# Optimization experiments

Hardware: AMD Instinct MI355X
Metric: run time of the kernel (lower is better)

Reference implementation:

```python
import jax, jax.numpy as jnp
import numpy as np

B, N, D = 16, 512, 256
PH, UH, UPH = 8, 4, 4          # P_GAT heads, U_GAT heads, UP_GAT heads
P_LAYERS, U_LAYERS = 2, 1
FH, NC = 128, 2                # final hidden, num classes
N_TRAIT = 4


def setup_inputs() -> dict:
    key = jax.random.key(0)
    keys = iter(jax.random.split(key, 64))

    def rn(shape, s=0.05):
        return jax.random.normal(next(keys), shape, dtype=jnp.float32) * s

    inp = {
        "p_mask": jnp.ones((B, N), jnp.float32),
        "feature": rn((B, N, D), 1.0),
        "c_node": rn((B, 1, D), 1.0),
        "pgat_W": rn((D, D)),
        "pgat_attn": rn((PH, 2 * (D // PH))),
    }
    for i in range(1, 5):
        inp[f"up{i}_qw"] = rn((D, D))
        inp[f"up{i}_qb"] = rn((D,))
        inp[f"up{i}_kw"] = rn((D, D))
        inp[f"up{i}_kb"] = rn((D,))
        inp[f"up{i}_ow"] = rn((D, D * UPH))
        inp[f"up{i}_ob"] = rn((D,))
    inp["ugat_W"] = rn((D, D))
    inp["ugat_attn"] = rn((UH, 2 * (D // UH)))
    inp["mlp_w1"] = rn((FH, D))
    inp["mlp_b1"] = rn((FH,))
    inp["mlp_w2"] = rn((FH, FH))
    inp["mlp_b2"] = rn((FH,))
    for i in range(1, 5):
        inp[f"fcf{i}_w"] = rn((NC, FH))
        inp[f"fcf{i}_b"] = rn((NC,))
    return inp


def _mh_gat(feature, W, attn_w, n_head, num_layers, adj=None):
    """Shared math of P_GAT / U_GAT.
    attn(cat([q_i, k_j]))[..., h, h] decomposes into q_i.wq_h + k_j.wk_h,
    identical math to the broadcast-concat-linear-diagonal in the source."""
    Bx, Nx, d = feature.shape
    dh = d // n_head
    wq, wk = attn_w[:, :dh], attn_w[:, dh:]           # [h, dh] each
    for _ in range(num_layers):
        qk = (feature @ W.T).reshape(Bx, Nx, n_head, dh)
        sq = jnp.einsum('bqhd,hd->bqh', qk, wq)
        sk = jnp.einsum('bkhd,hd->bkh', qk, wk)
        scores = jnp.tanh(sq[:, :, None, :] + sk[:, None, :, :])  # [B,q,k,h]
        if adj is not None:
            scores = jnp.where(adj[:, :, :, None] == 0, jnp.float32(-1e-8), scores)
        att = jax.nn.softmax(scores, axis=-2)          # softmax over k
        hid = jnp.tanh(jnp.einsum('bqkh,bkhd->bqhd', att, qk))
        feature = feature + hid.reshape(Bx, Nx, d)
    return feature


def _up_gat(p_mask, p_feat, u_feat, qw, qb, kw, kb, ow, ob):
    """UP_GAT: all heads/layers share params & inputs -> identical heads."""
    d = p_feat.shape[-1]
    q = u_feat @ qw.T + qb                             # [B,1,D]
    k = p_feat @ kw.T + kb                             # [B,Np,D]
    sim = jnp.einsum('bqd,bkd->bqk', q, k) / jnp.sqrt(jnp.float32(d))
    sim = jnp.where(p_mask[:, None, :] == 0, jnp.float32(1e-8), sim)
    att = jax.nn.softmax(sim, axis=2)
    head = att @ p_feat                                # [B,1,D]
    mh = jnp.concatenate([head] * UPH, axis=-1)        # concat of identical heads
    return (mh @ ow.T + ob)[:, 0, :]                   # squeeze(1)


def reference(p_mask, feature, c_node, pgat_W, pgat_attn,
              up1_qw, up1_qb, up1_kw, up1_kb, up1_ow, up1_ob,
              up2_qw, up2_qb, up2_kw, up2_kb, up2_ow, up2_ob,
              up3_qw, up3_qb, up3_kw, up3_kb, up3_ow, up3_ob,
              up4_qw, up4_qb, up4_kw, up4_kb, up4_ow, up4_ob,
              ugat_W, ugat_attn, mlp_w1, mlp_b1, mlp_w2, mlp_b2,
              fcf1_w, fcf1_b, fcf2_w, fcf2_b, fcf3_w, fcf3_b, fcf4_w, fcf4_b):
    Bx = p_mask.shape[0]
    adj = p_mask[:, :, None] * p_mask[:, None, :]      # [B,N,N]
    new_p = _mh_gat(feature, pgat_W, pgat_attn, PH, P_LAYERS, adj=adj)
    new_mask = jnp.concatenate([p_mask, jnp.ones((Bx, 1), p_mask.dtype)], axis=1)
    comb = jnp.concatenate([new_p, c_node], axis=1)    # [B,N+1,D]

    u1 = _up_gat(new_mask, comb, c_node, up1_qw, up1_qb, up1_kw, up1_kb, up1_ow, up1_ob)
    u2 = _up_gat(new_mask, comb, c_node, up2_qw, up2_qb, up2_kw, up2_kb, up2_ow, up2_ob)
    u3 = _up_gat(new_mask, comb, c_node, up3_qw, up3_qb, up3_kw, up3_kb, up3_ow, up3_ob)
    u4 = _up_gat(new_mask, comb, c_node, up4_qw, up4_qb, up4_kw, up4_kb, up4_ow, up4_ob)

    u = jnp.stack([u1, u2, u3, u4], axis=1)            # [B,4,D]
    u = _mh_gat(u, ugat_W, ugat_attn, UH, U_LAYERS, adj=None)

    def mlp(x):  # fcs1..4 share modules in the torch source
        h = jax.nn.relu(x @ mlp_w1.T + mlp_b1)
        return jax.nn.relu(h @ mlp_w2.T + mlp_b2)

    heads = [(fcf1_w, fcf1_b), (fcf2_w, fcf2_b), (fcf3_w, fcf3_b), (fcf4_w, fcf4_b)]
    logits = [mlp(u[:, i]) @ w.T + b for i, (w, b) in enumerate(heads)]
    return jnp.stack(logits, axis=0)                   # [4,B,NC]
```

## Files before the change

kernel.cpp:

```cpp
#include <hip/hip_runtime.h>

constexpr int CB   = 16;
constexpr int CN   = 512;
constexpr int CD   = 256;
constexpr int CPH  = 8;
constexpr int CDH  = 32;
constexpr int CNP1 = 513;
constexpr int CFH  = 128;
constexpr int CNC  = 2;

typedef __bf16 bf16x8 __attribute__((ext_vector_type(8)));
typedef __bf16 bf16x4 __attribute__((ext_vector_type(4)));
typedef float  f32x4  __attribute__((ext_vector_type(4)));

__device__ __forceinline__ float tanh_fast(float x) {
  x = fminf(fmaxf(x, -15.f), 15.f);
  float e = __expf(2.f * x);
  return (e - 1.f) / (e + 1.f);
}

__global__ __launch_bounds__(256) void gemm_fused(
    const float* __restrict__ A, const float* __restrict__ W,
    const float* __restrict__ attnw, __bf16* __restrict__ C,
    float* __restrict__ sqT, float* __restrict__ skT)
{
  const int t  = threadIdx.x;
  const int nt = blockIdx.x * 64;
  const int mt = blockIdx.y * 64;
  const int wv = t >> 6, ln = t & 63;
  const int quad = ln >> 4, lc = ln & 15;

  __shared__ __align__(16) __bf16 aHi[64][56];
  __shared__ __align__(16) __bf16 aLo[64][56];
  __shared__ __align__(16) __bf16 bHi[64][56];
  __shared__ __align__(16) __bf16 bLo[64][56];

  f32x4 acc[4];
#pragma unroll
  for (int j = 0; j < 4; j++)
#pragma unroll
    for (int r = 0; r < 4; r++) acc[j][r] = 0.f;

  const int sr  = t >> 2;
  const int skq = (t & 3) * 8;

  for (int k0 = 0; k0 < 256; k0 += 32) {
    __syncthreads();
    {
      const float* ap = A + (size_t)(mt + sr) * 256 + k0 + skq;
      const float* wp = W + (size_t)(nt + sr) * 256 + k0 + skq;
      float4 a0 = *(const float4*)ap, a1 = *(const float4*)(ap + 4);
      float4 w0 = *(const float4*)wp, w1 = *(const float4*)(wp + 4);
      float av[8] = {a0.x, a0.y, a0.z, a0.w, a1.x, a1.y, a1.z, a1.w};
      float wvv[8] = {w0.x, w0.y, w0.z, w0.w, w1.x, w1.y, w1.z, w1.w};
      bf16x8 ah, al, bh, bl;
#pragma unroll
      for (int j = 0; j < 8; j++) {
        ah[j] = (__bf16)av[j];
        al[j] = (__bf16)(av[j] - (float)ah[j]);
        bh[j] = (__bf16)wvv[j];
        bl[j] = (__bf16)(wvv[j] - (float)bh[j]);
      }
      *(bf16x8*)&aHi[sr][skq] = ah;
      *(bf16x8*)&aLo[sr][skq] = al;
      *(bf16x8*)&bHi[sr][skq] = bh;
      *(bf16x8*)&bLo[sr][skq] = bl;
    }
    __syncthreads();
    bf16x8 fah = *(const bf16x8*)&aHi[wv * 16 + lc][quad * 8];
    bf16x8 fal = *(const bf16x8*)&aLo[wv * 16 + lc][quad * 8];
#pragma unroll
    for (int j = 0; j < 4; j++) {
      bf16x8 fbh = *(const bf16x8*)&bHi[j * 16 + lc][quad * 8];
      bf16x8 fbl = *(const bf16x8*)&bLo[j * 16 + lc][quad * 8];
      acc[j] = __builtin_amdgcn_mfma_f32_16x16x32_bf16(fah, fbh, acc[j], 0, 0, 0);
      acc[j] = __builtin_amdgcn_mfma_f32_16x16x32_bf16(fah, fbl, acc[j], 0, 0, 0);
      acc[j] = __builtin_amdgcn_mfma_f32_16x16x32_bf16(fal, fbh, acc[j], 0, 0, 0);
    }
  }
#pragma unroll
  for (int j = 0; j < 4; j++)
#pragma unroll
    for (int r = 0; r < 4; r++)
      C[(size_t)(mt + wv * 16 + quad * 4 + r) * 256 + nt + j * 16 + lc] =
          (__bf16)acc[j][r];

  const int hA = blockIdx.x * 2, hB = hA + 1;
  const float wqa0 = attnw[hA * 64 + lc],      wqa1 = attnw[hA * 64 + 16 + lc];
  const float wka0 = attnw[hA * 64 + 32 + lc], wka1 = attnw[hA * 64 + 48 + lc];
  const float wqb0 = attnw[hB * 64 + lc],      wqb1 = attnw[hB * 64 + 16 + lc];
  const float wkb0 = attnw[hB * 64 + 32 + lc], wkb1 = attnw[hB * 64 + 48 + lc];
  float sqa[4], ska[4], sqb[4], skb[4];
#pragma unroll
  for (int r = 0; r < 4; r++) {
    sqa[r] = acc[0][r] * wqa0 + acc[1][r] * wqa1;
    ska[r] = acc[0][r] * wka0 + acc[1][r] * wka1;
    sqb[r] = acc[2][r] * wqb0 + acc[3][r] * wqb1;
    skb[r] = acc[2][r] * wkb0 + acc[3][r] * wkb1;
  }
#pragma unroll
  for (int m = 1; m <= 8; m <<= 1) {
#pragma unroll
    for (int r = 0; r < 4; r++) {
      sqa[r] += __shfl_xor(sqa[r], m);
      ska[r] += __shfl_xor(ska[r], m);
      sqb[r] += __shfl_xor(sqb[r], m);
      skb[r] += __shfl_xor(skb[r], m);
    }
  }
  if (lc == 0) {
#pragma unroll
    for (int r = 0; r < 4; r++) {
      int gm = mt + wv * 16 + quad * 4 + r;
      int bb = gm >> 9, nn = gm & 511;
      sqT[((size_t)bb * CPH + hA) * CN + nn] = sqa[r];
      skT[((size_t)bb * CPH + hA) * CN + nn] = ska[r];
      sqT[((size_t)bb * CPH + hB) * CN + nn] = sqb[r];
      skT[((size_t)bb * CPH + hB) * CN + nn] = skb[r];
    }
  }
}

__global__ __launch_bounds__(256) void pgat_attn_mfma(
    const __bf16* __restrict__ qk, const float* __restrict__ sqT,
    const float* __restrict__ skT, const float* __restrict__ pmask,
    const float* __restrict__ fin, float* __restrict__ fout, int outStride)
{
  const int qt = blockIdx.x;
  const int h  = blockIdx.y;
  const int b  = blockIdx.z;
  const int t  = threadIdx.x;
  const int wv = t >> 6;
  const int ln = t & 63;
  const int quad = ln >> 4;
  const int lc   = ln & 15;

  __shared__ __align__(16) __bf16 pbuf[64][72];
  __shared__ __align__(16) __bf16 vbuf[32][72];
  __shared__ float skl[CN];
  __shared__ float pml[CN];
  __shared__ float sql[64];
  __shared__ float pmq[64];

  for (int i = t; i < CN; i += 256) {
    skl[i] = skT[((size_t)b * CPH + h) * CN + i];
    pml[i] = pmask[b * CN + i];
  }
  if (t < 64) {
    sql[t] = sqT[((size_t)b * CPH + h) * CN + qt * 64 + t];
    pmq[t] = pmask[b * CN + qt * 64 + t];
  }

  f32x4 accV0 = {0.f, 0.f, 0.f, 0.f};
  f32x4 accV1 = {0.f, 0.f, 0.f, 0.f};
  f32x4 accD  = {0.f, 0.f, 0.f, 0.f};
  bf16x8 ones;
#pragma unroll
  for (int j = 0; j < 8; j++) ones[j] = (__bf16)1.0f;

  const int qg = t >> 2;
  const int kb = (t & 3) * 16;
  const int vkk = t >> 3;
  const int vdq = (t & 7) * 4;

  for (int k0 = 0; k0 < CN; k0 += 64) {
    __syncthreads();
    {
      bf16x4 v0 = *(const bf16x4*)(qk + ((size_t)(b * CN + k0 + vkk)) * CD + h * CDH + vdq);
      bf16x4 v1 = *(const bf16x4*)(qk + ((size_t)(b * CN + k0 + 32 + vkk)) * CD + h * CDH + vdq);
      vbuf[vdq + 0][vkk] = v0[0]; vbuf[vdq + 1][vkk] = v0[1];
      vbuf[vdq + 2][vkk] = v0[2]; vbuf[vdq + 3][vkk] = v0[3];
      vbuf[vdq + 0][32 + vkk] = v1[0]; vbuf[vdq + 1][32 + vkk] = v1[1];
      vbuf[vdq + 2][32 + vkk] = v1[2]; vbuf[vdq + 3][32 + vkk] = v1[3];
    }
    {
      float sq_ = sql[qg];
      float mq  = pmq[qg];
      bf16x8 w0, w1;
#pragma unroll
      for (int j = 0; j < 8; j++) {
        float s = tanh_fast(sq_ + skl[k0 + kb + j]);
        if (mq * pml[k0 + kb + j] == 0.f) s = -1e-8f;
        w0[j] = (__bf16)__expf(s);
      }
#pragma unroll
      for (int j = 0; j < 8; j++) {
        float s = tanh_fast(sq_ + skl[k0 + kb + 8 + j]);
        if (mq * pml[k0 + kb + 8 + j] == 0.f) s = -1e-8f;
        w1[j] = (__bf16)__expf(s);
      }
      *(bf16x8*)&pbuf[qg][kb]     = w0;
      *(bf16x8*)&pbuf[qg][kb + 8] = w1;
    }
    __syncthreads();
#pragma unroll
    for (int s = 0; s < 2; s++) {
      bf16x8 a  = *(const bf16x8*)&pbuf[wv * 16 + lc][s * 32 + quad * 8];
      bf16x8 b0 = *(const bf16x8*)&vbuf[lc][s * 32 + quad * 8];
      bf16x8 b1 = *(const bf16x8*)&vbuf[16 + lc][s * 32 + quad * 8];
      accV0 = __builtin_amdgcn_mfma_f32_16x16x32_bf16(a, b0, accV0, 0, 0, 0);
      accV1 = __builtin_amdgcn_mfma_f32_16x16x32_bf16(a, b1, accV1, 0, 0, 0);
      accD  = __builtin_amdgcn_mfma_f32_16x16x32_bf16(a, ones, accD, 0, 0, 0);
    }
  }
#pragma unroll
  for (int r = 0; r < 4; r++) {
    int q = qt * 64 + wv * 16 + quad * 4 + r;
    float inv = 1.f / accD[r];
    int d0 = h * CDH + lc;
    const float* ip = fin + ((size_t)b * CN + q) * CD;
    float*       op = fout + ((size_t)b * outStride + q) * CD;
    op[d0]      = ip[d0]      + tanh_fast(accV0[r] * inv);
    op[d0 + 16] = ip[d0 + 16] + tanh_fast(accV1[r] * inv);
  }
}


__global__ __launch_bounds__(256) void up_q_all(
    const float* __restrict__ cnode,
    const float* __restrict__ qw0, const float* __restrict__ qb0,
    const float* __restrict__ kw0, const float* __restrict__ kb0,
    const float* __restrict__ qw1, const float* __restrict__ qb1,
    const float* __restrict__ kw1, const float* __restrict__ kb1,
    const float* __restrict__ qw2, const float* __restrict__ qb2,
    const float* __restrict__ kw2, const float* __restrict__ kb2,
    const float* __restrict__ qw3, const float* __restrict__ qb3,
    const float* __restrict__ kw3, const float* __restrict__ kb3,
    float* __restrict__ qt_, float* __restrict__ qkb,
    float* __restrict__ comb, float* __restrict__ head, float* __restrict__ den)
{
  const int up = blockIdx.x, b = blockIdx.y, t = threadIdx.x;
  const float* qw = (up == 0) ? qw0 : (up == 1) ? qw1 : (up == 2) ? qw2 : qw3;
  const float* qb = (up == 0) ? qb0 : (up == 1) ? qb1 : (up == 2) ? qb2 : qb3;
  const float* kw = (up == 0) ? kw0 : (up == 1) ? kw1 : (up == 2) ? kw2 : kw3;
  const float* kb = (up == 0) ? kb0 : (up == 1) ? kb1 : (up == 2) ? kb2 : kb3;
  __shared__ float cl[CD];
  __shared__ float ql[CD];
  __shared__ float red[256];
  cl[t] = cnode[b * CD + t];
  head[((size_t)b * 4 + up) * CD + t] = 0.f;
  if (t == 0) den[b * 4 + up] = 0.f;
  __syncthreads();
  if (up == 0) comb[((size_t)b * CNP1 + CN) * CD + t] = cl[t];
  {
    const float* wr = qw + (size_t)t * CD;
    float a = qb[t];
#pragma unroll 4
    for (int k = 0; k < CD; k += 4) {
      float4 w4 = *(const float4*)(wr + k);
      a += cl[k] * w4.x + cl[k + 1] * w4.y + cl[k + 2] * w4.z + cl[k + 3] * w4.w;
    }
    ql[t] = a;
  }
  __syncthreads();
  {
    float a = 0.f;
    for (int d = 0; d < CD; d++) a += ql[d] * kw[d * CD + t];
    qt_[((size_t)up * CB + b) * CD + t] = a;
  }
  red[t] = ql[t] * kb[t];
  __syncthreads();
  for (int s = 128; s > 0; s >>= 1) { if (t < s) red[t] += red[t + s]; __syncthreads(); }
  if (t == 0) qkb[up * CB + b] = red[0];
}

__global__ __launch_bounds__(256) void up_headsim(
    const float* __restrict__ comb, const float* __restrict__ qt,
    const float* __restrict__ qkb, const float* __restrict__ pmask,
    float* __restrict__ head, float* __restrict__ den)
{
  const int b = blockIdx.x, n0 = blockIdx.y * 64, t = threadIdx.x;
  const int up = t >> 6, j = t & 63;
  __shared__ float qtl[4][CD];
  __shared__ float qkbl[4];
  __shared__ float attl[4][64];
  for (int i = t; i < 4 * CD; i += 256)
    qtl[i >> 8][i & 255] = qt[((size_t)(i >> 8) * CB + b) * CD + (i & 255)];
  if (t < 4) qkbl[t] = qkb[t * CB + b];
  __syncthreads();
  {
    const int n = n0 + j;
    float e = 0.f;
    if (n < CNP1) {
      const float* cr = comb + ((size_t)b * CNP1 + n) * CD;
      float p = 0.f;
#pragma unroll 4
      for (int d = 0; d < CD; d += 4) {
        float4 c4 = *(const float4*)(cr + d);
        p += qtl[up][d] * c4.x + qtl[up][d + 1] * c4.y
           + qtl[up][d + 2] * c4.z + qtl[up][d + 3] * c4.w;
      }
      float s = (p + qkbl[up]) * 0.0625f;
      float m = (n < CN) ? pmask[b * CN + n] : 1.f;
      if (m == 0.f) s = 1e-8f;
      e = __expf(s);
    }
    attl[up][j] = e;
  }
  __syncthreads();
  float4 acc = make_float4(0.f, 0.f, 0.f, 0.f);
  const int nmax = min(64, CNP1 - n0);
  for (int jj = 0; jj < nmax; jj++) {
    float a = attl[up][jj];
    float4 c4 = *(const float4*)(comb + ((size_t)b * CNP1 + n0 + jj) * CD + j * 4);
    acc.x += a * c4.x; acc.y += a * c4.y; acc.z += a * c4.z; acc.w += a * c4.w;
  }
  float* hp = head + ((size_t)b * 4 + up) * CD + j * 4;
  atomicAdd(hp + 0, acc.x); atomicAdd(hp + 1, acc.y);
  atomicAdd(hp + 2, acc.z); atomicAdd(hp + 3, acc.w);
  if (j == 0) {
    float s = 0.f;
    for (int jj = 0; jj < 64; jj++) s += attl[up][jj];
    atomicAdd(den + b * 4 + up, s);
  }
}

__global__ __launch_bounds__(256) void up_out_all(
    const float* __restrict__ head, const float* __restrict__ den,
    const float* __restrict__ ow0, const float* __restrict__ ob0,
    const float* __restrict__ ow1, const float* __restrict__ ob1,
    const float* __restrict__ ow2, const float* __restrict__ ob2,
    const float* __restrict__ ow3, const float* __restrict__ ob3,
    float* __restrict__ uout)
{
  const int b = blockIdx.x, up = blockIdx.y, t = threadIdx.x;
  const float* ow = (up == 0) ? ow0 : (up == 1) ? ow1 : (up == 2) ? ow2 : ow3;
  const float* ob = (up == 0) ? ob0 : (up == 1) ? ob1 : (up == 2) ? ob2 : ob3;
  __shared__ float hl[CD];
  hl[t] = head[((size_t)b * 4 + up) * CD + t] * (1.f / den[b * 4 + up]);
  __syncthreads();
  const float* r0 = ow + (size_t)t * 4 * CD;
  float a = ob[t];
#pragma unroll 2
  for (int dd = 0; dd < CD; dd += 4) {
    float4 w0 = *(const float4*)(r0 + dd);
    float4 w1 = *(const float4*)(r0 + CD + dd);
    float4 w2 = *(const float4*)(r0 + 2 * CD + dd);
    float4 w3 = *(const float4*)(r0 + 3 * CD + dd);
    a += hl[dd]     * (w0.x + w1.x + w2.x + w3.x)
       + hl[dd + 1] * (w0.y + w1.y + w2.y + w3.y)
       + hl[dd + 2] * (w0.z + w1.z + w2.z + w3.z)
       + hl[dd + 3] * (w0.w + w1.w + w2.w + w3.w);
  }
  uout[((size_t)b * 4 + up) * CD + t] = a;
}

__global__ __launch_bounds__(256) void ugat_qk(
    const float* __restrict__ u, const float* __restrict__ W,
    const float* __restrict__ attnw,
    float* __restrict__ uqk, float* __restrict__ sqk)
{
  const int b = blockIdx.x, node = blockIdx.y, t = threadIdx.x;
  __shared__ float ul[CD];
  __shared__ float qkl[CD];
  ul[t] = u[((size_t)b * 4 + node) * CD + t];
  __syncthreads();
  const float* wr = W + (size_t)t * CD;
  float p0 = 0.f, p1 = 0.f, p2 = 0.f, p3 = 0.f;
#pragma unroll 4
  for (int d = 0; d < CD; d += 16) {
    float4 w0 = *(const float4*)(wr + d);
    float4 w1 = *(const float4*)(wr + d + 4);
    float4 w2 = *(const float4*)(wr + d + 8);
    float4 w3 = *(const float4*)(wr + d + 12);
    p0 += ul[d +  0] * w0.x + ul[d +  1] * w0.y + ul[d +  2] * w0.z + ul[d +  3] * w0.w;
    p1 += ul[d +  4] * w1.x + ul[d +  5] * w1.y + ul[d +  6] * w1.z + ul[d +  7] * w1.w;
    p2 += ul[d +  8] * w2.x + ul[d +  9] * w2.y + ul[d + 10] * w2.z + ul[d + 11] * w2.w;
    p3 += ul[d + 12] * w3.x + ul[d + 13] * w3.y + ul[d + 14] * w3.z + ul[d + 15] * w3.w;
  }
  float a = (p0 + p1) + (p2 + p3);
  qkl[t] = a;
  uqk[((size_t)b * 4 + node) * CD + t] = a;
  __syncthreads();
  if (t < 8) {
    const int h = t >> 1, which = t & 1;
    const float* w = attnw + h * 128 + which * 64;
    float s = 0.f;
    for (int j = 0; j < 64; j++) s += qkl[h * 64 + j] * w[j];
    sqk[(((size_t)b * 4 + node) * 4 + h) * 2 + which] = s;
  }
}

__global__ __launch_bounds__(256) void ugat_mlp2(
    const float* __restrict__ u, const float* __restrict__ uqk,
    const float* __restrict__ sqk,
    const float* __restrict__ w1, const float* __restrict__ b1,
    const float* __restrict__ w2, const float* __restrict__ b2,
    const float* __restrict__ f1w, const float* __restrict__ f1b,
    const float* __restrict__ f2w, const float* __restrict__ f2b,
    const float* __restrict__ f3w, const float* __restrict__ f3b,
    const float* __restrict__ f4w, const float* __restrict__ f4b,
    float* __restrict__ out)
{
  const int b = blockIdx.x, trait = blockIdx.y, t = threadIdx.x;
  __shared__ float uq[4][CD];
  __shared__ float sl[4][4], kl[4][4];
  __shared__ float xl[CD];
  __shared__ float h1[CFH];
  __shared__ float h2[CFH];
  for (int i = t; i < 4 * CD; i += 256) uq[i >> 8][i & 255] = uqk[(size_t)b * 4 * CD + i];
  if (t < 16) {
    int node = t >> 2, h = t & 3;
    sl[node][h] = sqk[(((size_t)b * 4 + node) * 4 + h) * 2 + 0];
    kl[node][h] = sqk[(((size_t)b * 4 + node) * 4 + h) * 2 + 1];
  }
  float ur = u[((size_t)b * 4 + trait) * CD + t];
  __syncthreads();
  {
    const int h = t >> 6;
    float e[4]; float ssum = 0.f;
#pragma unroll
    for (int k = 0; k < 4; k++) { e[k] = __expf(tanh_fast(sl[trait][h] + kl[k][h])); ssum += e[k]; }
    float hid = 0.f;
#pragma unroll
    for (int k = 0; k < 4; k++) hid += e[k] * uq[k][t];
    xl[t] = ur + tanh_fast(hid / ssum);
  }
  __syncthreads();
  if (t < CFH) {
    const float* r = w1 + (size_t)t * CD;
    float a = b1[t];
#pragma unroll 4
    for (int k = 0; k < CD; k += 4) {
      float4 v = *(const float4*)(r + k);
      a += xl[k] * v.x + xl[k + 1] * v.y + xl[k + 2] * v.z + xl[k + 3] * v.w;
    }
    h1[t] = fmaxf(a, 0.f);
  }
  __syncthreads();
  if (t < CFH) {
    const float* r = w2 + (size_t)t * CFH;
    float a = b2[t];
#pragma unroll 4
    for (int k = 0; k < CFH; k += 4) {
      float4 v = *(const float4*)(r + k);
      a += h1[k] * v.x + h1[k + 1] * v.y + h1[k + 2] * v.z + h1[k + 3] * v.w;
    }
    h2[t] = fmaxf(a, 0.f);
  }
  __syncthreads();
  if (t < CNC) {
    const float* fw; const float* fb;
    switch (trait) {
      case 0:  fw = f1w; fb = f1b; break;
      case 1:  fw = f2w; fb = f2b; break;
      case 2:  fw = f3w; fb = f3b; break;
      default: fw = f4w; fb = f4b; break;
    }
    const float* r = fw + (size_t)t * CFH;
    float a = fb[t];
    for (int k = 0; k < CFH; k++) a += h2[k] * r[k];
    out[(size_t)trait * (CB * CNC) + b * CNC + t] = a;
  }
}

extern "C" void kernel_launch(void* const* d_in, const int* in_sizes, int n_in,
                              void* d_out, int out_size, void* d_ws, size_t ws_size,
                              hipStream_t stream) {
  (void)in_sizes; (void)n_in; (void)out_size; (void)ws_size;
  const float* pmask    = (const float*)d_in[0];
  const float* feature  = (const float*)d_in[1];
  const float* cnode    = (const float*)d_in[2];
  const float* pgat_W   = (const float*)d_in[3];
  const float* pgat_att = (const float*)d_in[4];
  const float* upw[4][6];
  for (int i = 0; i < 4; i++)
    for (int j = 0; j < 6; j++) upw[i][j] = (const float*)d_in[5 + i * 6 + j];
  const float* ugat_W   = (const float*)d_in[29];
  const float* ugat_att = (const float*)d_in[30];
  const float* mlp_w1 = (const float*)d_in[31];
  const float* mlp_b1 = (const float*)d_in[32];
  const float* mlp_w2 = (const float*)d_in[33];
  const float* mlp_b2 = (const float*)d_in[34];
  const float* fcf[8];
  for (int j = 0; j < 8; j++) fcf[j] = (const float*)d_in[35 + j];

  float* ws = (float*)d_ws;
  size_t o = 0;
  float* ws_qk   = ws + o; o += (size_t)CB * CN * CD;
  float* ws_feat = ws + o; o += (size_t)CB * CN * CD;
  float* ws_comb = ws + o; o += (size_t)CB * CNP1 * CD;
  float* ws_sq   = ws + o; o += (size_t)CB * CPH * CN;
  float* ws_sk   = ws + o; o += (size_t)CB * CPH * CN;
  float* ws_qt   = ws + o; o += (size_t)4 * CB * CD;
  float* ws_qkb  = ws + o; o += 4 * CB;
  float* ws_den  = ws + o; o += CB * 4;
  float* ws_head = ws + o; o += (size_t)CB * 4 * CD;
  float* ws_u    = ws + o; o += (size_t)CB * 4 * CD;
  float* ws_uqk  = ws + o; o += (size_t)CB * 4 * CD;
  float* ws_sqk  = ws + o; o += (size_t)CB * 4 * 4 * 2;
  __bf16* qk16 = (__bf16*)ws_qk;

  const dim3 gemmGrid(CD / 64, (CB * CN) / 64);
  const dim3 attnGrid(CN / 64, CPH, CB);

  gemm_fused<<<gemmGrid, 256, 0, stream>>>(feature, pgat_W, pgat_att, qk16, ws_sq, ws_sk);
  pgat_attn_mfma<<<attnGrid, 256, 0, stream>>>(qk16, ws_sq, ws_sk, pmask, feature, ws_feat, CN);
  gemm_fused<<<gemmGrid, 256, 0, stream>>>(ws_feat, pgat_W, pgat_att, qk16, ws_sq, ws_sk);
  pgat_attn_mfma<<<attnGrid, 256, 0, stream>>>(qk16, ws_sq, ws_sk, pmask, ws_feat, ws_comb, CNP1);

  up_q_all<<<dim3(4, CB), 256, 0, stream>>>(cnode,
      upw[0][0], upw[0][1], upw[0][2], upw[0][3],
      upw[1][0], upw[1][1], upw[1][2], upw[1][3],
      upw[2][0], upw[2][1], upw[2][2], upw[2][3],
      upw[3][0], upw[3][1], upw[3][2], upw[3][3],
      ws_qt, ws_qkb, ws_comb, ws_head, ws_den);
  up_headsim<<<dim3(CB, (CNP1 + 63) / 64), 256, 0, stream>>>(ws_comb, ws_qt, ws_qkb, pmask,
                                                             ws_head, ws_den);
  up_out_all<<<dim3(CB, 4), 256, 0, stream>>>(ws_head, ws_den,
      upw[0][4], upw[0][5], upw[1][4], upw[1][5],
      upw[2][4], upw[2][5], upw[3][4], upw[3][5], ws_u);

  ugat_qk<<<dim3(CB, 4), 256, 0, stream>>>(ws_u, ugat_W, ugat_att, ws_uqk, ws_sqk);
  ugat_mlp2<<<dim3(CB, 4), 256, 0, stream>>>(ws_u, ws_uqk, ws_sqk,
                                             mlp_w1, mlp_b1, mlp_w2, mlp_b2,
                                             fcf[0], fcf[1], fcf[2], fcf[3],
                                             fcf[4], fcf[5], fcf[6], fcf[7],
                                             (float*)d_out);
}
```

Before: 320.0 us.

## Factor tanh via exp products, enlarge attention query tile, fuse u-GAT qk kernel

The attention kernel precomputes exp(2*sq) and exp(2*sk) once per row and column, so each score needs one multiply, one reciprocal and one exp instead of a full tanh. The query tile grows from 64 to 128 per block so the staged V tile is reused by twice as many MFMAs, at the cost of more LDS and registers and half as many blocks. The UP_GAT output kernel is fused with the u-GAT qk projection to drop a launch, and an unroll pragma is added to one loop. The exp-product factoring with clamping can change numerics for large scores.

```diff
diff --git a/kernel.cpp b/kernel.cpp
--- a/kernel.cpp
+++ b/kernel.cpp
@@ -17,6 +17,11 @@
   x = fminf(fmaxf(x, -15.f), 15.f);
   float e = __expf(2.f * x);
   return (e - 1.f) / (e + 1.f);
+}
+
+__device__ __forceinline__ float exp2x_clamped(float x) {
+  x = fminf(fmaxf(x, -18.f), 18.f);
+  return __expf(2.f * x);
 }
 
 __global__ __launch_bounds__(256) void gemm_fused(
@@ -121,7 +126,7 @@
   }
 }
 
-__global__ __launch_bounds__(256) void pgat_attn_mfma(
+__global__ __launch_bounds__(256) void pgat_attn_mfma2(
     const __bf16* __restrict__ qk, const float* __restrict__ sqT,
     const float* __restrict__ skT, const float* __restrict__ pmask,
     const float* __restrict__ fin, float* __restrict__ fout, int outStride)
@@ -135,31 +140,30 @@
   const int quad = ln >> 4;
   const int lc   = ln & 15;
 
-  __shared__ __align__(16) __bf16 pbuf[64][72];
+  __shared__ __align__(16) __bf16 pbuf[128][72];
   __shared__ __align__(16) __bf16 vbuf[32][72];
   __shared__ float skl[CN];
   __shared__ float pml[CN];
-  __shared__ float sql[64];
-  __shared__ float pmq[64];
+  __shared__ float sql[128];
+  __shared__ float pmq[128];
 
   for (int i = t; i < CN; i += 256) {
-    skl[i] = skT[((size_t)b * CPH + h) * CN + i];
+    skl[i] = exp2x_clamped(skT[((size_t)b * CPH + h) * CN + i]);
     pml[i] = pmask[b * CN + i];
   }
-  if (t < 64) {
-    sql[t] = sqT[((size_t)b * CPH + h) * CN + qt * 64 + t];
-    pmq[t] = pmask[b * CN + qt * 64 + t];
-  }
-
-  f32x4 accV0 = {0.f, 0.f, 0.f, 0.f};
-  f32x4 accV1 = {0.f, 0.f, 0.f, 0.f};
-  f32x4 accD  = {0.f, 0.f, 0.f, 0.f};
+  if (t < 128) {
+    sql[t] = exp2x_clamped(sqT[((size_t)b * CPH + h) * CN + qt * 128 + t]);
+    pmq[t] = pmask[b * CN + qt * 128 + t];
+  }
+
+  f32x4 aV0 = {0.f,0.f,0.f,0.f}, aV1 = {0.f,0.f,0.f,0.f}, aD = {0.f,0.f,0.f,0.f};
+  f32x4 bV0 = {0.f,0.f,0.f,0.f}, bV1 = {0.f,0.f,0.f,0.f}, bD = {0.f,0.f,0.f,0.f};
   bf16x8 ones;
 #pragma unroll
   for (int j = 0; j < 8; j++) ones[j] = (__bf16)1.0f;
 
-  const int qg = t >> 2;
-  const int kb = (t & 3) * 16;
+  const int qg  = t >> 1;
+  const int kb  = (t & 1) * 32;
   const int vkk = t >> 3;
   const int vdq = (t & 7) * 4;
 
@@ -174,44 +178,57 @@
       vbuf[vdq + 2][32 + vkk] = v1[2]; vbuf[vdq + 3][32 + vkk] = v1[3];
     }
     {
-      float sq_ = sql[qg];
-      float mq  = pmq[qg];
-      bf16x8 w0, w1;
-#pragma unroll
-      for (int j = 0; j < 8; j++) {
-        float s = tanh_fast(sq_ + skl[k0 + kb + j]);
-        if (mq * pml[k0 + kb + j] == 0.f) s = -1e-8f;
-        w0[j] = (__bf16)__expf(s);
+      const float tq = sql[qg];
+      const float mq = pmq[qg];
+#pragma unroll
+      for (int g = 0; g < 4; g++) {
+        bf16x8 w;
+#pragma unroll
+        for (int j = 0; j < 8; j++) {
+          const int kk = k0 + kb + g * 8 + j;
+          float u  = fminf(tq * skl[kk], 1e30f);
+          float th = (u - 1.f) * __builtin_amdgcn_rcpf(u + 1.f);
+          float e  = __expf(th);
+          if (mq * pml[kk] == 0.f) e = 1.f;
+          w[j] = (__bf16)e;
+        }
+        *(bf16x8*)&pbuf[qg][kb + g * 8] = w;
       }
-#pragma unroll
-      for (int j = 0; j < 8; j++) {
-        float s = tanh_fast(sq_ + skl[k0 + kb + 8 + j]);
-        if (mq * pml[k0 + kb + 8 + j] == 0.f) s = -1e-8f;
-        w1[j] = (__bf16)__expf(s);
-      }
-      *(bf16x8*)&pbuf[qg][kb]     = w0;
-      *(bf16x8*)&pbuf[qg][kb + 8] = w1;
     }
     __syncthreads();
 #pragma unroll
     for (int s = 0; s < 2; s++) {
-      bf16x8 a  = *(const bf16x8*)&pbuf[wv * 16 + lc][s * 32 + quad * 8];
       bf16x8 b0 = *(const bf16x8*)&vbuf[lc][s * 32 + quad * 8];
       bf16x8 b1 = *(const bf16x8*)&vbuf[16 + lc][s * 32 + quad * 8];
-      accV0 = __builtin_amdgcn_mfma_f32_16x16x32_bf16(a, b0, accV0, 0, 0, 0);
-      accV1 = __builtin_amdgcn_mfma_f32_16x16x32_bf16(a, b1, accV1, 0, 0, 0);
-      accD  = __builtin_amdgcn_mfma_f32_16x16x32_bf16(a, ones, accD, 0, 0, 0);
+      bf16x8 fa = *(const bf16x8*)&pbuf[wv * 16 + lc][s * 32 + quad * 8];
+      bf16x8 fb = *(const bf16x8*)&pbuf[64 + wv * 16 + lc][s * 32 + quad * 8];
+      aV0 = __builtin_amdgcn_mfma_f32_16x16x32_bf16(fa, b0, aV0, 0, 0, 0);
+      aV1 = __builtin_amdgcn_mfma_f32_16x16x32_bf16(fa, b1, aV1, 0, 0, 0);
+      aD  = __builtin_amdgcn_mfma_f32_16x16x32_bf16(fa, ones, aD, 0, 0, 0);
+      bV0 = __builtin_amdgcn_mfma_f32_16x16x32_bf16(fb, b0, bV0, 0, 0, 0);
+      bV1 = __builtin_amdgcn_mfma_f32_16x16x32_bf16(fb, b1, bV1, 0, 0, 0);
+      bD  = __builtin_amdgcn_mfma_f32_16x16x32_bf16(fb, ones, bD, 0, 0, 0);
     }
   }
 #pragma unroll
   for (int r = 0; r < 4; r++) {
-    int q = qt * 64 + wv * 16 + quad * 4 + r;
-    float inv = 1.f / accD[r];
-    int d0 = h * CDH + lc;
-    const float* ip = fin + ((size_t)b * CN + q) * CD;
-    float*       op = fout + ((size_t)b * outStride + q) * CD;
-    op[d0]      = ip[d0]      + tanh_fast(accV0[r] * inv);
-    op[d0 + 16] = ip[d0 + 16] + tanh_fast(accV1[r] * inv);
+    const int d0 = h * CDH + lc;
+    {
+      int q = qt * 128 + wv * 16 + quad * 4 + r;
+      float inv = 1.f / aD[r];
+      const float* ip = fin + ((size_t)b * CN + q) * CD;
+      float*       op = fout + ((size_t)b * outStride + q) * CD;
+      op[d0]      = ip[d0]      + tanh_fast(aV0[r] * inv);
+      op[d0 + 16] = ip[d0 + 16] + tanh_fast(aV1[r] * inv);
+    }
+    {
+      int q = qt * 128 + 64 + wv * 16 + quad * 4 + r;
+      float inv = 1.f / bD[r];
+      const float* ip = fin + ((size_t)b * CN + q) * CD;
+      float*       op = fout + ((size_t)b * outStride + q) * CD;
+      op[d0]      = ip[d0]      + tanh_fast(bV0[r] * inv);
+      op[d0 + 16] = ip[d0 + 16] + tanh_fast(bV1[r] * inv);
+    }
   }
 }
 
@@ -255,6 +272,7 @@
   __syncthreads();
   {
     float a = 0.f;
+#pragma unroll 8
     for (int d = 0; d < CD; d++) a += ql[d] * kw[d * CD + t];
     qt_[((size_t)up * CB + b) * CD + t] = a;
   }
@@ -315,69 +333,66 @@
   }
 }
 
-__global__ __launch_bounds__(256) void up_out_all(
+__global__ __launch_bounds__(256) void up_out_ugat(
     const float* __restrict__ head, const float* __restrict__ den,
     const float* __restrict__ ow0, const float* __restrict__ ob0,
     const float* __restrict__ ow1, const float* __restrict__ ob1,
     const float* __restrict__ ow2, const float* __restrict__ ob2,
     const float* __restrict__ ow3, const float* __restrict__ ob3,
-    float* __restrict__ uout)
+    const float* __restrict__ ugat_W, const float* __restrict__ attnw,
+    float* __restrict__ uout, float* __restrict__ uqk, float* __restrict__ sqk)
 {
   const int b = blockIdx.x, up = blockIdx.y, t = threadIdx.x;
   const float* ow = (up == 0) ? ow0 : (up == 1) ? ow1 : (up == 2) ? ow2 : ow3;
   const float* ob = (up == 0) ? ob0 : (up == 1) ? ob1 : (up == 2) ? ob2 : ob3;
   __shared__ float hl[CD];
+  __shared__ float xl[CD];
+  __shared__ float qkl[CD];
   hl[t] = head[((size_t)b * 4 + up) * CD + t] * (1.f / den[b * 4 + up]);
   __syncthreads();
-  const float* r0 = ow + (size_t)t * 4 * CD;
-  float a = ob[t];
+  {
+    const float* r0 = ow + (size_t)t * 4 * CD;
+    float a = ob[t];
 #pragma unroll 2
-  for (int dd = 0; dd < CD; dd += 4) {
-    float4 w0 = *(const float4*)(r0 + dd);
-    float4 w1 = *(const float4*)(r0 + CD + dd);
-    float4 w2 = *(const float4*)(r0 + 2 * CD + dd);
-    float4 w3 = *(const float4*)(r0 + 3 * CD + dd);
-    a += hl[dd]     * (w0.x + w1.x + w2.x + w3.x)
-       + hl[dd + 1] * (w0.y + w1.y + w2.y + w3.y)
-       + hl[dd + 2] * (w0.z + w1.z + w2.z + w3.z)
-       + hl[dd + 3] * (w0.w + w1.w + w2.w + w3.w);
-  }
-  uout[((size_t)b * 4 + up) * CD + t] = a;
-}
-
-__global__ __launch_bounds__(256) void ugat_qk(
-    const float* __restrict__ u, const float* __restrict__ W,
-    const float* __restrict__ attnw,
-    float* __restrict__ uqk, float* __restrict__ sqk)
-{
-  const int b = blockIdx.x, node = blockIdx.y, t = threadIdx.x;
-  __shared__ float ul[CD];
-  __shared__ float qkl[CD];
-  ul[t] = u[((size_t)b * 4 + node) * CD + t];
-  __syncthreads();
-  const float* wr = W + (size_t)t * CD;
-  float p0 = 0.f, p1 = 0.f, p2 = 0.f, p3 = 0.f;
+    for (int dd = 0; dd < CD; dd += 4) {
+      float4 w0 = *(const float4*)(r0 + dd);
+      float4 w1 = *(const float4*)(r0 + CD + dd);
+      float4 w2 = *(const float4*)(r0 + 2 * CD + dd);
+      float4 w3 = *(const float4*)(r0 + 3 * CD + dd);
+      a += hl[dd]     * (w0.x + w1.x + w2.x + w3.x)
+         + hl[dd + 1] * (w0.y + w1.y + w2.y + w3.y)
+         + hl[dd + 2] * (w0.z + w1.z + w2.z + w3.z)
+         + hl[dd + 3] * (w0.w + w1.w + w2.w + w3.w);
+    }
+    xl[t] = a;
+    uout[((size_t)b * 4 + up) * CD + t] = a;
+  }
+  __syncthreads();
+  {
+    const float* wr = ugat_W + (size_t)t * CD;
+    float p0 = 0.f, p1 = 0.f, p2 = 0.f, p3 = 0.f;
 #pragma unroll 4
-  for (int d = 0; d < CD; d += 16) {
-    float4 w0 = *(const float4*)(wr + d);
-    float4 w1 = *(const float4*)(wr + d + 4);
-    float4 w2 = *(const float4*)(wr + d + 8);
-    float4 w3 = *(const float4*)(wr + d + 12);
-    p0 += ul[d +  0] * w0.x + ul[d +  1] * w0.y + ul[d +  2] * w0.z + ul[d +  3] * w0.w;
-    p1 += ul[d +  4] * w1.x + ul[d +  5] * w1.y + ul[d +  6] * w1.z + ul[d +  7] * w1.w;
-    p2 += ul[d +  8] * w2.x + ul[d +  9] * w2.y + ul[d + 10] * w2.z + ul[d + 11] * w2.w;
-    p3 += ul[d + 12] * w3.x + ul[d + 13] * w3.y + ul[d + 14] * w3.z + ul[d + 15] * w3.w;
-  }
-  float a = (p0 + p1) + (p2 + p3);
-  qkl[t] = a;
-  uqk[((size_t)b * 4 + node) * CD + t] = a;
+    for (int d = 0; d < CD; d += 16) {
+      float4 w0 = *(const float4*)(wr + d);
+      float4 w1 = *(const float4*)(wr + d + 4);
+      float4 w2 = *(const float4*)(wr + d + 8);
+      float4 w3 = *(const float4*)(wr + d + 12);
+      p0 += xl[d +  0] * w0.x + xl[d +  1] * w0.y + xl[d +  2] * w0.z + xl[d +  3] * w0.w;
+      p1 += xl[d +  4] * w1.x + xl[d +  5] * w1.y + xl[d +  6] * w1.z + xl[d +  7] * w1.w;
+      p2 += xl[d +  8] * w2.x + xl[d +  9] * w2.y + xl[d + 10] * w2.z + xl[d + 11] * w2.w;
+      p3 += xl[d + 12] * w3.x + xl[d + 13] * w3.y + xl[d + 14] * w3.z + xl[d + 15] * w3.w;
+    }
+    float a = (p0 + p1) + (p2 + p3);
+    qkl[t] = a;
+    uqk[((size_t)b * 4 + up) * CD + t] = a;
+  }
   __syncthreads();
   if (t < 8) {
     const int h = t >> 1, which = t & 1;
     const float* w = attnw + h * 128 + which * 64;
     float s = 0.f;
     for (int j = 0; j < 64; j++) s += qkl[h * 64 + j] * w[j];
-    sqk[(((size_t)b * 4 + node) * 4 + h) * 2 + which] = s;
+    sqk[(((size_t)b * 4 + up) * 4 + h) * 2 + which] = s;
   }
 }
 
@@ -492,12 +507,12 @@
   __bf16* qk16 = (__bf16*)ws_qk;
 
   const dim3 gemmGrid(CD / 64, (CB * CN) / 64);
-  const dim3 attnGrid(CN / 64, CPH, CB);
+  const dim3 attnGrid(CN / 128, CPH, CB);
 
   gemm_fused<<<gemmGrid, 256, 0, stream>>>(feature, pgat_W, pgat_att, qk16, ws_sq, ws_sk);
-  pgat_attn_mfma<<<attnGrid, 256, 0, stream>>>(qk16, ws_sq, ws_sk, pmask, feature, ws_feat, CN);
+  pgat_attn_mfma2<<<attnGrid, 256, 0, stream>>>(qk16, ws_sq, ws_sk, pmask, feature, ws_feat, CN);
   gemm_fused<<<gemmGrid, 256, 0, stream>>>(ws_feat, pgat_W, pgat_att, qk16, ws_sq, ws_sk);
-  pgat_attn_mfma<<<attnGrid, 256, 0, stream>>>(qk16, ws_sq, ws_sk, pmask, ws_feat, ws_comb, CNP1);
+  pgat_attn_mfma2<<<attnGrid, 256, 0, stream>>>(qk16, ws_sq, ws_sk, pmask, ws_feat, ws_comb, CNP1);
 
   up_q_all<<<dim3(4, CB), 256, 0, stream>>>(cnode,
       upw[0][0], upw[0][1], upw[0][2], upw[0][3],
@@ -507,11 +522,11 @@
       ws_qt, ws_qkb, ws_comb, ws_head, ws_den);
   up_headsim<<<dim3(CB, (CNP1 + 63) / 64), 256, 0, stream>>>(ws_comb, ws_qt, ws_qkb, pmask,
                                                              ws_head, ws_den);
-  up_out_all<<<dim3(CB, 4), 256, 0, stream>>>(ws_head, ws_den,
+  up_out_ugat<<<dim3(CB, 4), 256, 0, stream>>>(ws_head, ws_den,
       upw[0][4], upw[0][5], upw[1][4], upw[1][5],
-      upw[2][4], upw[2][5], upw[3][4], upw[3][5], ws_u);
-
-  ugat_qk<<<dim3(CB, 4), 256, 0, stream>>>(ws_u, ugat_W, ugat_att, ws_uqk, ws_sqk);
+      upw[2][4], upw[2][5], upw[3][4], upw[3][5],
+      ugat_W, ugat_att, ws_u, ws_uqk, ws_sqk);
+
   ugat_mlp2<<<dim3(CB, 4), 256, 0, stream>>>(ws_u, ws_uqk, ws_sqk,
                                              mlp_w1, mlp_b1, mlp_w2, mlp_b2,
                                              fcf[0], fcf[1], fcf[2], fcf[3],
```

New measurement: 302.0 us. 5.6% less time.
